# Kernel tuning notes

Hardware: AMD Instinct MI355X
Metric: run time of the kernel (lower is better)

## Reference

```python
import jax, jax.numpy as jnp
import numpy as np

HEAD_SIZE = 128


def setup_inputs() -> dict:
    key = jax.random.key(0)
    k0, k1, k2, k3 = jax.random.split(key, 4)
    B, S, E, H = 4, 4096, 1024, HEAD_SIZE
    x = jax.random.normal(k0, (B, S, E), dtype=jnp.float32)
    scale = 1.0 / np.sqrt(E).astype(np.float32)
    Wq = jax.random.normal(k1, (E, H), dtype=jnp.float32) * scale
    Wk = jax.random.normal(k2, (E, H), dtype=jnp.float32) * scale
    Wv = jax.random.normal(k3, (E, H), dtype=jnp.float32) * scale
    k_mask = jnp.ones((B, S), dtype=jnp.int32)
    return {"x": x, "Wq": Wq, "Wk": Wk, "Wv": Wv, "k_mask": k_mask}


def reference(x, Wq, Wk, Wv, k_mask):
    # Self-attention path (kv=None), causal=True
    Q = x @ Wq  # [B, S, H]
    K = x @ Wk  # [B, S, H]
    V = x @ Wv  # [B, S, H]
    inv_sqrt_h = np.float32(1.0 / np.sqrt(HEAD_SIZE))
    att = jnp.einsum('bqh,bkh->bqk', Q, K) * inv_sqrt_h  # [B, S, S]
    neg_inf = jnp.float32(-jnp.inf)
    # padding mask over keys: [B, 1, S_k]
    att = jnp.where(k_mask[:, None, :] == 0, neg_inf, att)
    # causal mask: tril over (q_len, k_len)
    S = Q.shape[1]
    c_mask = jnp.tril(jnp.ones((S, S), dtype=bool))  # [S, S]
    att = jnp.where(c_mask[None, :, :], att, neg_inf)
    att = jax.nn.softmax(att, axis=-1)
    return att @ V  # [B, S, H]
```

## Files before the change

### kernel.cpp

```cpp
#include <hip/hip_runtime.h>
#include <hip/hip_bf16.h>

typedef unsigned short u16;
typedef __attribute__((ext_vector_type(8))) short bf16x8;
typedef __attribute__((ext_vector_type(4))) float f32x4;
typedef __attribute__((ext_vector_type(4))) unsigned short u16x4;

#define SQ 4096
#define HQ 128
#define NCHUNK 144

__device__ __forceinline__ u16 f2b(float f) {
  unsigned int u = __float_as_uint(f);
  unsigned int r = (u + 0x7fffu + ((u >> 16) & 1u)) >> 16;
  return (u16)r;
}

__device__ __forceinline__ u16 f2b_fast(float f) {
  __hip_bfloat16 h = __float2bfloat16(f);
  return __builtin_bit_cast(u16, h);
}

__device__ __forceinline__ float b2f(u16 v) {
  unsigned int u = ((unsigned int)v) << 16;
  return __uint_as_float(u);
}

__device__ __forceinline__ void gload_lds16(const u16* gsrc, u16* ldst) {
  __builtin_amdgcn_global_load_lds((const __attribute__((address_space(1))) void*)gsrc,
                                   (__attribute__((address_space(3))) void*)ldst, 16, 0, 0);
}

__global__ __launch_bounds__(256) void k_wt(const float* __restrict__ Wq, const float* __restrict__ Wk,
                                            const float* __restrict__ Wv, u16* __restrict__ wt) {
  int idx = blockIdx.x * 256 + threadIdx.x;
  int z = idx >> 17, r = idx & 131071, n = r >> 10, k = r & 1023;
  const float* W = (z == 0) ? Wq : (z == 1) ? Wk : Wv;
  wt[idx] = f2b(W[k * 128 + n]);
}

__global__ __launch_bounds__(512, 4) void k_proj(const float* __restrict__ x, const u16* __restrict__ wt,
                                                 u16* __restrict__ qb, u16* __restrict__ kb,
                                                 u16* __restrict__ vt) {
  int mt = blockIdx.x, nh = blockIdx.y;
  int t = threadIdx.x;
  int w = t >> 6, lane = t & 63;
  int wm = w >> 2, wn = w & 3;
  int lr = lane & 15, lg = lane >> 4;

  __shared__ __align__(16) u16 xl[2][64 * 32];
  __shared__ __align__(16) u16 wl[2][192 * 32];

  int srow = t >> 3, sc8 = t & 7;
  const float* xg = x + (long)(mt * 64 + srow) * 1024 + sc8 * 4;
  int xch = ((sc8 >> 1) ^ ((srow >> 1) & 3));
  int xoff = srow * 32 + xch * 8 + (sc8 & 1) * 4;

  f32x4 acc[2][3];
#pragma unroll
  for (int i = 0; i < 2; ++i)
#pragma unroll
    for (int j = 0; j < 3; ++j) acc[i][j] = (f32x4){0.f, 0.f, 0.f, 0.f};

  const u16* wbase = wt + (long)(nh * 192) * 1024;

  auto stage_w = [&](int bufi, int k0) {
#pragma unroll
    for (int i = 0; i < 2; ++i) {
      int ci = i * 512 + t;
      if (ci < 768) {
        int row = ci >> 2, ch = ci & 3;
        gload_lds16(wbase + (long)row * 1024 + k0 + ((ch ^ ((row >> 1) & 3)) << 3),
                    &wl[bufi][0] + ci * 8);
      }
    }
  };

  auto xwrite = [&](int bufi, float4 a, float4 b2) {
    u16x4 o0, o1;
    o0[0] = f2b_fast(a.x); o0[1] = f2b_fast(a.y); o0[2] = f2b_fast(a.z); o0[3] = f2b_fast(a.w);
    o1[0] = f2b_fast(b2.x); o1[1] = f2b_fast(b2.y); o1[2] = f2b_fast(b2.z); o1[3] = f2b_fast(b2.w);
    *(u16x4*)(&xl[bufi][0] + xoff) = (sc8 & 1) ? o0 : o0;
  };

  {
    float4 a0 = *(const float4*)(xg);
    stage_w(0, 0);
    u16x4 o;
    o[0] = f2b_fast(a0.x); o[1] = f2b_fast(a0.y); o[2] = f2b_fast(a0.z); o[3] = f2b_fast(a0.w);
    *(u16x4*)(&xl[0][0] + xoff) = o;
  }
  float4 p0 = *(const float4*)(xg + 32);
  float4 p1 = *(const float4*)(xg + 64);
  __syncthreads();

  for (int ks = 0; ks < 32; ++ks) {
    int cur = ks & 1;
    float4 p2;
    if (ks + 3 < 32) p2 = *(const float4*)(xg + (ks + 3) * 32);
    if (ks + 1 < 32) {
      stage_w(cur ^ 1, (ks + 1) * 32);
      u16x4 o;
      o[0] = f2b_fast(p0.x); o[1] = f2b_fast(p0.y); o[2] = f2b_fast(p0.z); o[3] = f2b_fast(p0.w);
      *(u16x4*)(&xl[cur ^ 1][0] + xoff) = o;
    }
    bf16x8 af[2], bfr[3];
#pragma unroll
    for (int i = 0; i < 2; ++i) {
      int row = wm * 32 + i * 16 + lr;
      af[i] = *(const bf16x8*)(&xl[cur][0] + row * 32 + ((lg ^ ((row >> 1) & 3)) << 3));
    }
#pragma unroll
    for (int j = 0; j < 3; ++j) {
      int row = wn * 48 + j * 16 + lr;
      bfr[j] = *(const bf16x8*)(&wl[cur][0] + row * 32 + ((lg ^ ((row >> 1) & 3)) << 3));
    }
#pragma unroll
    for (int i = 0; i < 2; ++i)
#pragma unroll
      for (int j = 0; j < 3; ++j)
        acc[i][j] = __builtin_amdgcn_mfma_f32_16x16x32_bf16(af[i], bfr[j], acc[i][j], 0, 0, 0);
    p0 = p1; p1 = p2;
    __syncthreads();
  }

#pragma unroll
  for (int i = 0; i < 2; ++i)
#pragma unroll
    for (int j = 0; j < 3; ++j)
#pragma unroll
      for (int r = 0; r < 4; ++r) {
        int m = mt * 64 + wm * 32 + i * 16 + lg * 4 + r;
        int col = nh * 192 + wn * 48 + j * 16 + lr;
        int z = col >> 7, cz = col & 127;
        u16 v = f2b(acc[i][j][r]);
        if (z == 0) qb[(long)m * 128 + cz] = v;
        else if (z == 1) kb[(long)m * 128 + cz] = v;
        else { int bb = m >> 12, sR = m & 4095; vt[(long)bb * 524288 + (long)cz * 4096 + sR] = v; }
      }
}

__global__ __launch_bounds__(512, 4) void k_attn(const u16* __restrict__ qb, const u16* __restrict__ kb,
                                                 const u16* __restrict__ vt, const int* __restrict__ kmask,
                                                 u16* __restrict__ po, float* __restrict__ pl) {
  const float SCALE_LOG2 = 0.08838834764831845f * 1.4426950408889634f;
  const float MFIX = 24.0f;
  int f = (NCHUNK - 1) - (int)blockIdx.x;
  int b = blockIdx.y;
  int qt2 = 0, cum = 0;
  while (cum + ((qt2 + 4) >> 2) <= f) { cum += (qt2 + 4) >> 2; ++qt2; }
  int kc = f - cum;
  int ntile = 2 * qt2 + 2;
  int kt0 = kc * 8;
  int kt1 = min(kt0 + 8, ntile);

  int t = threadIdx.x, w = t >> 6, lane = t & 63;
  int lr = lane & 15, lg = lane >> 4, sw = lr & 7;
  int qrow0 = qt2 * 128 + w * 16;
  const u16* Q = qb + ((long)(b * SQ + qrow0)) * HQ;
  const u16* K = kb + (long)b * SQ * HQ;
  const u16* V = vt + (long)b * HQ * SQ;
  const int* msk = kmask + b * SQ;

  __shared__ __align__(16) u16 Kl[2][64 * 128];
  __shared__ __align__(16) u16 Vl[2][128 * 64];
  __shared__ __align__(16) u16 plds[8][16 * 64];

  bf16x8 aq[4];
#pragma unroll
  for (int c = 0; c < 4; ++c) aq[c] = *(const bf16x8*)(Q + lr * HQ + c * 32 + lg * 8);

  bf16x8 ones;
#pragma unroll
  for (int e = 0; e < 8; ++e) ones[e] = (short)0x3F80;

  f32x4 o[8];
#pragma unroll
  for (int n = 0; n < 8; ++n) o[n] = (f32x4){0.f, 0.f, 0.f, 0.f};
  f32x4 l_acc = (f32x4){0.f, 0.f, 0.f, 0.f};

  auto stage = [&](int bufi, int kb0) {
    const u16* Kg = K + (long)kb0 * HQ;
    const u16* Vg = V + kb0;
#pragma unroll
    for (int i = 0; i < 2; ++i) {
      int ci = w * 2 + i;
      int o16 = ci * 64 + lane;
      int row = o16 >> 4, ch = o16 & 15;
      gload_lds16(Kg + row * HQ + ((ch ^ (row & 7)) << 3), &Kl[bufi][ci * 512]);
    }
#pragma unroll
    for (int i = 0; i < 2; ++i) {
      int ci = w * 2 + i;
      int o16 = ci * 64 + lane;
      int row = o16 >> 3, ch = o16 & 7;
      gload_lds16(Vg + (long)row * SQ + ((ch ^ (row & 7)) << 3), &Vl[bufi][ci * 512]);
    }
  };

  stage(0, kt0 * 64);
  __syncthreads();

  u16* pw = &plds[w][0];
  for (int kt = kt0; kt < kt1; ++kt) {
    int cur = (kt - kt0) & 1;
    int kb0 = kt * 64;
    if (kt + 1 < kt1) stage(cur ^ 1, kb0 + 64);

    if (kb0 <= qrow0 + 15) {
      f32x4 s[4];
#pragma unroll
      for (int h = 0; h < 4; ++h) {
        f32x4 acc = (f32x4){0.f, 0.f, 0.f, 0.f};
        const u16* Kp = &Kl[cur][(h * 16 + lr) * 128];
#pragma unroll
        for (int c = 0; c < 4; ++c) {
          bf16x8 bk = *(const bf16x8*)(Kp + (((c * 4 + lg) ^ sw) << 3));
          acc = __builtin_amdgcn_mfma_f32_16x16x32_bf16(aq[c], bk, acc, 0, 0, 0);
        }
        s[h] = acc;
      }
      float mf[4];
#pragma unroll
      for (int h = 0; h < 4; ++h) mf[h] = (msk[kb0 + h * 16 + lr] != 0) ? 1.0f : 0.0f;
      bool needc = (kb0 + 63 > qrow0);
#pragma unroll
      for (int r = 0; r < 4; ++r) {
        int row = lg * 4 + r;
        int qr = qrow0 + row;
#pragma unroll
        for (int h = 0; h < 4; ++h) {
          float p = __builtin_exp2f(fmaf(s[h][r], SCALE_LOG2, -MFIX)) * mf[h];
          if (needc) p = ((kb0 + h * 16 + lr) <= qr) ? p : 0.0f;
          int poff = row * 64 + ((((h * 2 + (lr >> 3)) ^ (row & 7))) << 3) + (lr & 7);
          pw[poff] = f2b_fast(p);
        }
      }
      bf16x8 ap0 = *(const bf16x8*)(pw + lr * 64 + ((lg ^ sw) << 3));
      bf16x8 ap1 = *(const bf16x8*)(pw + lr * 64 + (((4 + lg) ^ sw) << 3));
      l_acc = __builtin_amdgcn_mfma_f32_16x16x32_bf16(ap0, ones, l_acc, 0, 0, 0);
      l_acc = __builtin_amdgcn_mfma_f32_16x16x32_bf16(ap1, ones, l_acc, 0, 0, 0);
#pragma unroll
      for (int n = 0; n < 8; ++n) {
        const u16* Vp = &Vl[cur][(n * 16 + lr) * 64];
        bf16x8 bv0 = *(const bf16x8*)(Vp + ((lg ^ sw) << 3));
        bf16x8 bv1 = *(const bf16x8*)(Vp + (((4 + lg) ^ sw) << 3));
        o[n] = __builtin_amdgcn_mfma_f32_16x16x32_bf16(ap0, bv0, o[n], 0, 0, 0);
        o[n] = __builtin_amdgcn_mfma_f32_16x16x32_bf16(ap1, bv1, o[n], 0, 0, 0);
      }
    }
    __syncthreads();
  }

  long p = (long)b * NCHUNK + f;
  u16* pob = po + p * 16384;
#pragma unroll
  for (int n = 0; n < 8; ++n)
#pragma unroll
    for (int r = 0; r < 4; ++r)
      pob[(w * 16 + lg * 4 + r) * 128 + n * 16 + lr] = f2b_fast(o[n][r]);
  if (lr == 0) {
#pragma unroll
    for (int r = 0; r < 4; ++r) pl[p * 128 + w * 16 + lg * 4 + r] = l_acc[r];
  }
}

__global__ __launch_bounds__(256) void k_merge(const u16* __restrict__ po, const float* __restrict__ pl,
                                               float* __restrict__ out) {
  int qt2 = blockIdx.x, b = blockIdx.y;
  int nch = (qt2 + 4) >> 2;
  int pre = 0;
  for (int q = 0; q < qt2; ++q) pre += (q + 4) >> 2;
  long pbase = (long)b * NCHUNK + pre;
  int t = threadIdx.x;
  int row = t >> 1, c0 = (t & 1) * 64;
  float l = 0.f;
  for (int i = 0; i < nch; ++i) l += pl[(pbase + i) * 128 + row];
  float inv = 1.0f / l;
  const u16* p0 = po + pbase * 16384 + row * 128 + c0;
  float* orow = out + ((long)(b * SQ + qt2 * 128 + row)) * HQ + c0;
#pragma unroll
  for (int j = 0; j < 64; j += 4) {
    float acc0 = 0.f, acc1 = 0.f, acc2 = 0.f, acc3 = 0.f;
    for (int i = 0; i < nch; ++i) {
      u16x4 v = *(const u16x4*)(p0 + (long)i * 16384 + j);
      acc0 += b2f(v[0]); acc1 += b2f(v[1]); acc2 += b2f(v[2]); acc3 += b2f(v[3]);
    }
    float4 r = {acc0 * inv, acc1 * inv, acc2 * inv, acc3 * inv};
    *(float4*)(orow + j) = r;
  }
}

extern "C" void kernel_launch(void* const* d_in, const int* in_sizes, int n_in,
                              void* d_out, int out_size, void* d_ws, size_t ws_size,
                              hipStream_t stream) {
  const float* x  = (const float*)d_in[0];
  const float* Wq = (const float*)d_in[1];
  const float* Wk = (const float*)d_in[2];
  const float* Wv = (const float*)d_in[3];
  const int* kmask = (const int*)d_in[4];
  char* ws = (char*)d_ws;
  u16* wt = (u16*)(ws + 33554432);
  u16* qb = (u16*)(ws + 34340864);
  u16* kb = (u16*)(ws + 38535168);
  u16* vt = (u16*)(ws + 42729472);
  u16* po = (u16*)ws;
  float* pl = (float*)(ws + 31195136);
  float* out = (float*)d_out;

  k_wt<<<1536, 256, 0, stream>>>(Wq, Wk, Wv, wt);
  k_proj<<<dim3(256, 2), 512, 0, stream>>>(x, wt, qb, kb, vt);
  k_attn<<<dim3(NCHUNK, 4), 512, 0, stream>>>(qb, kb, vt, kmask, po, pl);
  k_merge<<<dim3(32, 4), 256, 0, stream>>>(po, pl, out);
}
```

Before: 117.4 us.

## Retile projection GEMM and stream fp32 x into LDS via async loads

The projection kernel now uses 128x96 output tiles with 256 threads (4 waves, each 64x48) instead of 64x192 tiles with 512 threads. The fp32 activations are copied straight into LDS with global_load_lds using an XOR swizzle and converted to bf16 only when fragments are read, replacing the register prefetch with convert-and-store. This is meant to hide x-load latency with async copies and cut VALU and register-staging overhead. In exchange it doubles A-tile LDS footprint (fp32) and re-reads x twice as many times across N blocks (4 instead of 2), with conversion repeated per wave.

```diff
diff --git a/kernel.cpp b/kernel.cpp
--- a/kernel.cpp
+++ b/kernel.cpp
@@ -26,7 +26,7 @@
   return __uint_as_float(u);
 }
 
-__device__ __forceinline__ void gload_lds16(const u16* gsrc, u16* ldst) {
+__device__ __forceinline__ void gload_lds16(const void* gsrc, void* ldst) {
   __builtin_amdgcn_global_load_lds((const __attribute__((address_space(1))) void*)gsrc,
                                    (__attribute__((address_space(3))) void*)ldst, 16, 0, 0);
 }
@@ -39,99 +39,97 @@
   wt[idx] = f2b(W[k * 128 + n]);
 }
 
-__global__ __launch_bounds__(512, 4) void k_proj(const float* __restrict__ x, const u16* __restrict__ wt,
-                                                 u16* __restrict__ qb, u16* __restrict__ kb,
-                                                 u16* __restrict__ vt) {
+__global__ __launch_bounds__(256) void k_proj(const float* __restrict__ x, const u16* __restrict__ wt,
+                                              u16* __restrict__ qb, u16* __restrict__ kb,
+                                              u16* __restrict__ vt) {
   int mt = blockIdx.x, nh = blockIdx.y;
   int t = threadIdx.x;
   int w = t >> 6, lane = t & 63;
-  int wm = w >> 2, wn = w & 3;
+  int wm = w >> 1, wn = w & 1;
   int lr = lane & 15, lg = lane >> 4;
 
-  __shared__ __align__(16) u16 xl[2][64 * 32];
-  __shared__ __align__(16) u16 wl[2][192 * 32];
-
-  int srow = t >> 3, sc8 = t & 7;
-  const float* xg = x + (long)(mt * 64 + srow) * 1024 + sc8 * 4;
-  int xch = ((sc8 >> 1) ^ ((srow >> 1) & 3));
-  int xoff = srow * 32 + xch * 8 + (sc8 & 1) * 4;
-
-  f32x4 acc[2][3];
-#pragma unroll
-  for (int i = 0; i < 2; ++i)
+  __shared__ __align__(16) float Al[2][128 * 32];
+  __shared__ __align__(16) u16 Bl[2][96 * 32];
+
+  f32x4 acc[4][3];
+#pragma unroll
+  for (int i = 0; i < 4; ++i)
 #pragma unroll
     for (int j = 0; j < 3; ++j) acc[i][j] = (f32x4){0.f, 0.f, 0.f, 0.f};
 
-  const u16* wbase = wt + (long)(nh * 192) * 1024;
-
-  auto stage_w = [&](int bufi, int k0) {
-#pragma unroll
-    for (int i = 0; i < 2; ++i) {
-      int ci = i * 512 + t;
-      if (ci < 768) {
-        int row = ci >> 2, ch = ci & 3;
-        gload_lds16(wbase + (long)row * 1024 + k0 + ((ch ^ ((row >> 1) & 3)) << 3),
-                    &wl[bufi][0] + ci * 8);
-      }
+  const float* xbase = x + (long)(mt * 128) * 1024;
+  const u16* wbase = wt + (long)(nh * 96) * 1024;
+
+  auto stage_a = [&](int bufi, int k0) {
+#pragma unroll
+    for (int i = 0; i < 4; ++i) {
+      int ci = i * 256 + t;
+      int row = ci >> 3, ch = ci & 7;
+      gload_lds16(xbase + (long)row * 1024 + k0 + ((ch ^ (row & 7)) << 2),
+                  &Al[bufi][0] + ci * 4);
     }
   };
-
-  auto xwrite = [&](int bufi, float4 a, float4 b2) {
-    u16x4 o0, o1;
-    o0[0] = f2b_fast(a.x); o0[1] = f2b_fast(a.y); o0[2] = f2b_fast(a.z); o0[3] = f2b_fast(a.w);
-    o1[0] = f2b_fast(b2.x); o1[1] = f2b_fast(b2.y); o1[2] = f2b_fast(b2.z); o1[3] = f2b_fast(b2.w);
-    *(u16x4*)(&xl[bufi][0] + xoff) = (sc8 & 1) ? o0 : o0;
+  auto stage_b = [&](int bufi, int k0) {
+    {
+      int ci = t;
+      int row = ci >> 2, ch = ci & 3;
+      gload_lds16(wbase + (long)row * 1024 + k0 + ((ch ^ ((row >> 1) & 3)) << 3),
+                  &Bl[bufi][0] + ci * 8);
+    }
+    if (t < 128) {
+      int ci = 256 + t;
+      int row = ci >> 2, ch = ci & 3;
+      gload_lds16(wbase + (long)row * 1024 + k0 + ((ch ^ ((row >> 1) & 3)) << 3),
+                  &Bl[bufi][0] + ci * 8);
+    }
   };
 
-  {
-    float4 a0 = *(const float4*)(xg);
-    stage_w(0, 0);
-    u16x4 o;
-    o[0] = f2b_fast(a0.x); o[1] = f2b_fast(a0.y); o[2] = f2b_fast(a0.z); o[3] = f2b_fast(a0.w);
-    *(u16x4*)(&xl[0][0] + xoff) = o;
-  }
-  float4 p0 = *(const float4*)(xg + 32);
-  float4 p1 = *(const float4*)(xg + 64);
+  stage_a(0, 0);
+  stage_b(0, 0);
   __syncthreads();
 
   for (int ks = 0; ks < 32; ++ks) {
     int cur = ks & 1;
-    float4 p2;
-    if (ks + 3 < 32) p2 = *(const float4*)(xg + (ks + 3) * 32);
     if (ks + 1 < 32) {
-      stage_w(cur ^ 1, (ks + 1) * 32);
-      u16x4 o;
-      o[0] = f2b_fast(p0.x); o[1] = f2b_fast(p0.y); o[2] = f2b_fast(p0.z); o[3] = f2b_fast(p0.w);
-      *(u16x4*)(&xl[cur ^ 1][0] + xoff) = o;
-    }
-    bf16x8 af[2], bfr[3];
-#pragma unroll
-    for (int i = 0; i < 2; ++i) {
-      int row = wm * 32 + i * 16 + lr;
-      af[i] = *(const bf16x8*)(&xl[cur][0] + row * 32 + ((lg ^ ((row >> 1) & 3)) << 3));
+      stage_a(cur ^ 1, (ks + 1) * 32);
+      stage_b(cur ^ 1, (ks + 1) * 32);
+    }
+    bf16x8 af[4], bfr[3];
+#pragma unroll
+    for (int i = 0; i < 4; ++i) {
+      int row = wm * 64 + i * 16 + lr;
+      const float* Ap = &Al[cur][row * 32];
+      int sz = row & 7;
+      float4 fa = *(const float4*)(Ap + (((2 * lg) ^ sz) << 2));
+      float4 fb = *(const float4*)(Ap + (((2 * lg + 1) ^ sz) << 2));
+      bf16x8 v;
+      v[0] = (short)f2b_fast(fa.x); v[1] = (short)f2b_fast(fa.y);
+      v[2] = (short)f2b_fast(fa.z); v[3] = (short)f2b_fast(fa.w);
+      v[4] = (short)f2b_fast(fb.x); v[5] = (short)f2b_fast(fb.y);
+      v[6] = (short)f2b_fast(fb.z); v[7] = (short)f2b_fast(fb.w);
+      af[i] = v;
     }
 #pragma unroll
     for (int j = 0; j < 3; ++j) {
       int row = wn * 48 + j * 16 + lr;
-      bfr[j] = *(const bf16x8*)(&wl[cur][0] + row * 32 + ((lg ^ ((row >> 1) & 3)) << 3));
-    }
-#pragma unroll
-    for (int i = 0; i < 2; ++i)
+      bfr[j] = *(const bf16x8*)(&Bl[cur][0] + row * 32 + ((lg ^ ((row >> 1) & 3)) << 3));
+    }
+#pragma unroll
+    for (int i = 0; i < 4; ++i)
 #pragma unroll
       for (int j = 0; j < 3; ++j)
         acc[i][j] = __builtin_amdgcn_mfma_f32_16x16x32_bf16(af[i], bfr[j], acc[i][j], 0, 0, 0);
-    p0 = p1; p1 = p2;
     __syncthreads();
   }
 
 #pragma unroll
-  for (int i = 0; i < 2; ++i)
+  for (int i = 0; i < 4; ++i)
 #pragma unroll
     for (int j = 0; j < 3; ++j)
 #pragma unroll
       for (int r = 0; r < 4; ++r) {
-        int m = mt * 64 + wm * 32 + i * 16 + lg * 4 + r;
-        int col = nh * 192 + wn * 48 + j * 16 + lr;
+        int m = mt * 128 + wm * 64 + i * 16 + lg * 4 + r;
+        int col = nh * 96 + wn * 48 + j * 16 + lr;
         int z = col >> 7, cz = col & 127;
         u16 v = f2b(acc[i][j][r]);
         if (z == 0) qb[(long)m * 128 + cz] = v;
@@ -309,7 +307,7 @@
   float* out = (float*)d_out;
 
   k_wt<<<1536, 256, 0, stream>>>(Wq, Wk, Wv, wt);
-  k_proj<<<dim3(256, 2), 512, 0, stream>>>(x, wt, qb, kb, vt);
+  k_proj<<<dim3(128, 4), 256, 0, stream>>>(x, wt, qb, kb, vt);
   k_attn<<<dim3(NCHUNK, 4), 512, 0, stream>>>(qb, kb, vt, kmask, po, pl);
   k_merge<<<dim3(32, 4), 256, 0, stream>>>(po, pl, out);
 }
```

New measurement: 125.7 us. +7.0%, slower.
